# Optimization experiments

Hardware: AMD Instinct MI355X
Metric: run time of the kernel (lower is better)

## Reference

```python
import jax, jax.numpy as jnp
import numpy as np

NUM_HEADS = 8
NUM_LANDMARKS = 64
TOPK_LANDMARKS = 4


def setup_inputs() -> dict:
    key = jax.random.key(0)
    k1, k2, k3, k4 = jax.random.split(key, 4)
    B, N, C = 1, 2048, 512
    return {
        "x": jax.random.normal(k1, (B, N, C), jnp.float32),
        "w_qkv": jax.random.normal(k2, (3 * C, C), jnp.float32) * 0.02,
        "w_proj": jax.random.normal(k3, (C, C), jnp.float32) * 0.02,
        "b_proj": jax.random.normal(k4, (C,), jnp.float32) * 0.02,
    }


def reference(x, w_qkv, w_proj, b_proj):
    B, N, C = x.shape
    H = NUM_HEADS
    Dh = C // H
    m = min(NUM_LANDMARKS, N)          # number of segments (torch views (B,H,m,seg,D))
    kl = min(TOPK_LANDMARKS, m)
    scale = Dh ** -0.5

    qkv = (x @ w_qkv.T).reshape(B, N, 3, H, Dh).transpose(2, 0, 3, 1, 4)
    q, k, v = qkv[0], qkv[1], qkv[2]   # each (B,H,N,Dh)

    seg = -(-N // m)                   # segment length = ceil(N/m)
    pad = seg * m - N

    def segmentize(t):
        if pad > 0:
            t = jnp.pad(t, ((0, 0), (0, 0), (0, pad), (0, 0)))
        return t.reshape(B, H, m, seg, Dh)

    k_seg = segmentize(k)              # (B,H,m,seg,Dh)
    v_seg = segmentize(v)

    centroids = k_seg.mean(axis=3)     # (B,H,m,Dh) -- includes pad zeros, as in torch
    route = jnp.einsum('bhnd,bhmd->bhnm', q, centroids) * scale
    _, topk_idx = jax.lax.top_k(route, kl)  # (B,H,N,kl)

    # gather routed segments per query: (B,H,N,kl,seg,Dh)
    gather = jax.vmap(jax.vmap(lambda segs, ix: segs[ix]))
    sel_k = gather(k_seg, topk_idx).reshape(B, H, N, kl * seg, Dh)
    sel_v = gather(v_seg, topk_idx).reshape(B, H, N, kl * seg, Dh)

    attn = jnp.einsum('bhnd,bhnkd->bhnk', q, sel_k) * scale
    attn = jax.nn.softmax(attn, axis=-1)
    out = jnp.einsum('bhnk,bhnkd->bhnd', attn, sel_v)  # (B,H,N,Dh)
    out = out.transpose(0, 2, 1, 3).reshape(B, N, C)
    return out @ w_proj.T + b_proj
```

## Files before the change

kernel.cpp:

```cpp
#include <hip/hip_runtime.h>
#include <hip/hip_bf16.h>
#include <math.h>

#define N_TOK 2048
#define C_DIM 512
#define H_NUM 8
#define DH 64
#define M_LM 64
#define SEG 32
#define KL 4
#define SCALE 0.125f

typedef __attribute__((ext_vector_type(8))) short short8;
typedef __attribute__((ext_vector_type(8))) unsigned short ushort8v;
typedef __attribute__((ext_vector_type(4))) float f32x4;

__device__ inline unsigned short f2bf(float f) {
  unsigned u = __float_as_uint(f);
  u += 0x7FFF + ((u >> 16) & 1);
  return (unsigned short)(u >> 16);
}
__device__ inline float bf2f(unsigned short h) {
  return __uint_as_float(((unsigned)h) << 16);
}

__global__ __launch_bounds__(256) void gemm_qk(
    const float* __restrict__ A, const float* __restrict__ B,
    float* __restrict__ out_q, float* __restrict__ out_k,
    unsigned short* __restrict__ kbf)
{
  __shared__ float As[2][32][68];
  __shared__ float Bs[2][32][68];
  int tid = threadIdx.x;
  int tx = tid & 15, ty = tid >> 4;
  int row0 = blockIdx.y << 6;
  int col0 = blockIdx.x << 6;
  float acc[4][4] = {};
  int kk = tid & 31, rr = tid >> 5;

  float pa[8], pb[8];
#pragma unroll
  for (int i = 0; i < 8; i++) {
    pa[i] = A[(size_t)(row0 + rr + i * 8) * 512 + kk];
    pb[i] = B[(size_t)(col0 + rr + i * 8) * 512 + kk];
  }
#pragma unroll
  for (int i = 0; i < 8; i++) {
    As[0][kk][rr + i * 8] = pa[i];
    Bs[0][kk][rr + i * 8] = pb[i];
  }
  __syncthreads();

  for (int t = 0; t < 16; t++) {
    int cur = t & 1;
    if (t + 1 < 16) {
#pragma unroll
      for (int i = 0; i < 8; i++) {
        pa[i] = A[(size_t)(row0 + rr + i * 8) * 512 + (t + 1) * 32 + kk];
        pb[i] = B[(size_t)(col0 + rr + i * 8) * 512 + (t + 1) * 32 + kk];
      }
    }
#pragma unroll
    for (int kk2 = 0; kk2 < 32; kk2++) {
      float a[4], b[4];
      *(float4*)a = *(const float4*)&As[cur][kk2][ty << 2];
      *(float4*)b = *(const float4*)&Bs[cur][kk2][tx << 2];
#pragma unroll
      for (int i = 0; i < 4; i++)
#pragma unroll
        for (int j = 0; j < 4; j++) acc[i][j] += a[i] * b[j];
    }
    if (t + 1 < 16) {
#pragma unroll
      for (int i = 0; i < 8; i++) {
        As[cur ^ 1][kk][rr + i * 8] = pa[i];
        Bs[cur ^ 1][kk][rr + i * 8] = pb[i];
      }
    }
    __syncthreads();
  }

  int t = col0 >> 9;
  int h = (col0 >> 6) & 7;
  float* dst = (t == 0) ? out_q : out_k;
#pragma unroll
  for (int i = 0; i < 4; i++) {
    int n = row0 + (ty << 2) + i;
#pragma unroll
    for (int j = 0; j < 4; j++) {
      int d = (tx << 2) + j;
      float v = acc[i][j];
      dst[(size_t)((h << 11) + n) * DH + d] = v;
      if (t == 1) kbf[(size_t)((h << 11) + n) * DH + d] = f2bf(v);
    }
  }
}

__global__ void split3_kernel(const float* __restrict__ x, const float* __restrict__ wv,
                              const float* __restrict__ wp,
                              unsigned short* __restrict__ X2,
                              unsigned short* __restrict__ W2v,
                              unsigned short* __restrict__ WP2)
{
  int idx = blockIdx.x * 256 + threadIdx.x;
  const float* src; unsigned short* dst; int li;
  if (idx < 1048576)      { src = x;  dst = X2;  li = idx; }
  else if (idx < 1310720) { src = wv; dst = W2v; li = idx - 1048576; }
  else                    { src = wp; dst = WP2; li = idx - 1310720; }
  int r = li >> 9, k = li & 511;
  float a = src[li];
  unsigned short h1 = f2bf(a);
  float r1 = a - bf2f(h1);
  dst[(size_t)(r << 10) + k] = h1;
  dst[(size_t)(r << 10) + 512 + k] = f2bf(r1);
}

__global__ __launch_bounds__(256) void gemm_mfma(
    const unsigned short* __restrict__ A2, const unsigned short* __restrict__ B2,
    unsigned short* __restrict__ ov16, float* __restrict__ ofull,
    const float* __restrict__ bias, int ldout, int mode)
{
  __shared__ short Al[4096];
  __shared__ short Bl[4096];
  int tid = threadIdx.x;
  int lane = tid & 63, w = tid >> 6;
  int row0 = blockIdx.y << 6, col0 = blockIdx.x << 6;
  int wr = (w >> 1) * 32, wc = (w & 1) * 32;
  int m_lo = tid & 7, h8 = (tid >> 3) & 7, m_hi = tid >> 6;
  int ms = m_hi * 8 + m_lo;
  int q = lane >> 4, ln = lane & 15;

  f32x4 acc[2][2];
#pragma unroll
  for (int mi = 0; mi < 2; mi++)
#pragma unroll
    for (int ni = 0; ni < 2; ni++)
#pragma unroll
      for (int r = 0; r < 4; r++) acc[mi][ni][r] = 0.0f;

  for (int s = 0; s < 24; s++) {
    int ka = (s < 8) ? s * 64 : (s < 16) ? 512 + (s - 8) * 64 : (s - 16) * 64;
    int kb = (s < 8) ? s * 64 : (s < 16) ? (s - 8) * 64 : 512 + (s - 16) * 64;
    short8 a0 = *(const short8*)(A2 + (size_t)(row0 + ms) * 1024 + ka + h8 * 8);
    short8 a1 = *(const short8*)(A2 + (size_t)(row0 + ms + 32) * 1024 + ka + h8 * 8);
    short8 b0 = *(const short8*)(B2 + (size_t)(col0 + ms) * 1024 + kb + h8 * 8);
    short8 b1 = *(const short8*)(B2 + (size_t)(col0 + ms + 32) * 1024 + kb + h8 * 8);
    __syncthreads();
    *(short8*)&Al[(h8 * 64 + ms) * 8] = a0;
    *(short8*)&Al[(h8 * 64 + ms + 32) * 8] = a1;
    *(short8*)&Bl[(h8 * 64 + ms) * 8] = b0;
    *(short8*)&Bl[(h8 * 64 + ms + 32) * 8] = b1;
    __syncthreads();
    short8 af[2][2], bf[2][2];
#pragma unroll
    for (int sub = 0; sub < 2; sub++)
#pragma unroll
      for (int i = 0; i < 2; i++) {
        af[sub][i] = *(const short8*)&Al[((sub * 4 + q) * 64 + wr + i * 16 + ln) * 8];
        bf[sub][i] = *(const short8*)&Bl[((sub * 4 + q) * 64 + wc + i * 16 + ln) * 8];
      }
#pragma unroll
    for (int sub = 0; sub < 2; sub++)
#pragma unroll
      for (int mi = 0; mi < 2; mi++)
#pragma unroll
        for (int ni = 0; ni < 2; ni++)
          acc[mi][ni] = __builtin_amdgcn_mfma_f32_16x16x32_bf16(
              af[sub][mi], bf[sub][ni], acc[mi][ni], 0, 0, 0);
  }

  if (mode == 0) {
    int hh = (col0 >> 6) & 7;
#pragma unroll
    for (int mi = 0; mi < 2; mi++)
#pragma unroll
      for (int ni = 0; ni < 2; ni++)
#pragma unroll
        for (int r = 0; r < 4; r++) {
          int row = row0 + wr + mi * 16 + q * 4 + r;
          int d = wc + ni * 16 + ln;
          ov16[(size_t)((hh << 11) + row) * DH + d] = f2bf(acc[mi][ni][r]);
        }
  } else {
#pragma unroll
    for (int mi = 0; mi < 2; mi++)
#pragma unroll
      for (int ni = 0; ni < 2; ni++)
#pragma unroll
        for (int r = 0; r < 4; r++) {
          int row = row0 + wr + mi * 16 + q * 4 + r;
          int col = col0 + wc + ni * 16 + ln;
          ofull[(size_t)row * ldout + col] = acc[mi][ni][r] + bias[col];
        }
  }
}

__global__ void centroid_kernel(const float* __restrict__ kb, float* __restrict__ cent)
{
  int idx = blockIdx.x * blockDim.x + threadIdx.x;
  int m = (idx >> 6) & 63;
  int h = idx >> 12;
  int d = idx & 63;
  const float* base = kb + ((size_t)(h << 11) + m * SEG) * DH + d;
  float s = 0.f;
#pragma unroll
  for (int ss = 0; ss < SEG; ss++) s += base[(size_t)ss * DH];
  cent[idx] = s * (1.0f / SEG);
}

__global__ __launch_bounds__(256) void route_topk_kernel(
    const float* __restrict__ qb, const float* __restrict__ cent, int* __restrict__ topk)
{
  __shared__ float centT[64][65];
  __shared__ float qs[4][64];
  int tid = threadIdx.x;
  int wave = tid >> 6, lane = tid & 63;
  int qi = (blockIdx.x << 2) + wave;
  int h = qi >> 11;
  qs[wave][lane] = qb[(size_t)qi * DH + lane];
  const float4* c4 = (const float4*)(cent + ((size_t)h << 12));
#pragma unroll
  for (int i = 0; i < 4; i++) {
    int f4 = tid + 256 * i;
    int m = f4 >> 4;
    int d0 = (f4 & 15) * 4;
    float4 v = c4[f4];
    centT[d0][m] = v.x; centT[d0 + 1][m] = v.y;
    centT[d0 + 2][m] = v.z; centT[d0 + 3][m] = v.w;
  }
  __syncthreads();
  float dot = 0.f;
#pragma unroll
  for (int d = 0; d < 64; d++) dot += qs[wave][d] * centT[d][lane];
  float val = dot * SCALE;
  for (int r = 0; r < KL; r++) {
    float v = val;
    int id = lane;
#pragma unroll
    for (int off = 32; off; off >>= 1) {
      float ov = __shfl_xor(v, off, 64);
      int oi = __shfl_xor(id, off, 64);
      if (ov > v || (ov == v && oi < id)) { v = ov; id = oi; }
    }
    if (lane == 0) topk[qi * KL + r] = id;
    if (lane == id) val = -INFINITY;
  }
}

__global__ __launch_bounds__(256) void attn_kernel(
    const float* __restrict__ qb, const unsigned short* __restrict__ kbf,
    const unsigned short* __restrict__ vbf, const int* __restrict__ topk,
    unsigned short* __restrict__ ao2)
{
  __shared__ float probs[4][132];
  int tid = threadIdx.x;
  int wave = tid >> 6, lane = tid & 63;
  int qi = (blockIdx.x << 2) + wave;
  int h = qi >> 11, n = qi & 2047;
  int4 tk = *(const int4*)(topk + qi * KL);
  int segArr[4] = {tk.x, tk.y, tk.z, tk.w};
  const float* qrow = qb + (size_t)qi * DH;
  float4 qreg[4];
#pragma unroll
  for (int j = 0; j < 2; j++) {
    qreg[j * 2]     = *(const float4*)(qrow + ((lane & 3) + 4 * j) * 8);
    qreg[j * 2 + 1] = *(const float4*)(qrow + ((lane & 3) + 4 * j) * 8 + 4);
  }

  float e[8];
  float score[8];
#pragma unroll
  for (int g = 0; g < 8; g++) {
    int seg = segArr[g >> 1];
    int key_n = seg * SEG + (lane >> 2) + 16 * (g & 1);
    const unsigned short* krow = kbf + ((size_t)(h << 11) + key_n) * DH;
    float a0 = 0.f, a1 = 0.f, a2 = 0.f, a3 = 0.f;
#pragma unroll
    for (int j = 0; j < 2; j++) {
      ushort8v kv = *(const ushort8v*)(krow + ((lane & 3) + 4 * j) * 8);
      float4 q0 = qreg[j * 2], q1 = qreg[j * 2 + 1];
      a0 += q0.x * bf2f(kv[0]); a1 += q0.y * bf2f(kv[1]);
      a2 += q0.z * bf2f(kv[2]); a3 += q0.w * bf2f(kv[3]);
      a0 += q1.x * bf2f(kv[4]); a1 += q1.y * bf2f(kv[5]);
      a2 += q1.z * bf2f(kv[6]); a3 += q1.w * bf2f(kv[7]);
    }
    float acc = (a0 + a1) + (a2 + a3);
    acc += __shfl_xor(acc, 1, 64);
    acc += __shfl_xor(acc, 2, 64);
    score[g] = acc * SCALE;
  }
  float mx = score[0];
#pragma unroll
  for (int g = 1; g < 8; g++) mx = fmaxf(mx, score[g]);
#pragma unroll
  for (int off = 4; off < 64; off <<= 1) mx = fmaxf(mx, __shfl_xor(mx, off, 64));
  float ls = 0.f;
#pragma unroll
  for (int g = 0; g < 8; g++) { e[g] = expf(score[g] - mx); ls += e[g]; }
#pragma unroll
  for (int off = 4; off < 64; off <<= 1) ls += __shfl_xor(ls, off, 64);
  float inv = 1.0f / ls;
  if ((lane & 3) == 0) {
#pragma unroll
    for (int g = 0; g < 8; g++)
      probs[wave][(g >> 1) * 33 + (lane >> 2) + 16 * (g & 1)] = e[g] * inv;
  }
  __syncthreads();

  int gi = lane >> 4, lx = lane & 15;
  int rh = lx >> 3, dl = lx & 7;
  int seg = segArr[gi];
  const unsigned short* vbase = vbf + ((size_t)(h << 11) + seg * SEG) * DH + dl * 8;
  float o[8] = {};
#pragma unroll
  for (int ss = 0; ss < 16; ss++) {
    int row = rh * 16 + ss;
    float p = probs[wave][gi * 33 + row];
    ushort8v vv = *(const ushort8v*)(vbase + (size_t)row * DH);
#pragma unroll
    for (int j = 0; j < 8; j++) o[j] += p * bf2f(vv[j]);
  }
#pragma unroll
  for (int off = 8; off < 64; off <<= 1) {
#pragma unroll
    for (int j = 0; j < 8; j++) o[j] += __shfl_xor(o[j], off, 64);
  }
  if (lane < 8) {
    ushort8v hi8, lo8;
#pragma unroll
    for (int j = 0; j < 8; j++) {
      unsigned short hb = f2bf(o[j]);
      hi8[j] = (short)hb;
      lo8[j] = (short)f2bf(o[j] - bf2f(hb));
    }
    *(ushort8v*)(ao2 + (size_t)n * 1024 + (h << 6) + (lane << 3)) = hi8;
    *(ushort8v*)(ao2 + (size_t)n * 1024 + 512 + (h << 6) + (lane << 3)) = lo8;
  }
}

extern "C" void kernel_launch(void* const* d_in, const int* in_sizes, int n_in,
                              void* d_out, int out_size, void* d_ws, size_t ws_size,
                              hipStream_t stream)
{
  const float* x      = (const float*)d_in[0];
  const float* w_qkv  = (const float*)d_in[1];
  const float* w_proj = (const float*)d_in[2];
  const float* b_proj = (const float*)d_in[3];
  float* out = (float*)d_out;

  float* base = (float*)d_ws;
  float* qbuf = base;
  float* kbuf = base + 1048576;
  unsigned short* vbf = (unsigned short*)(base + 2097152);
  unsigned short* kbf = (unsigned short*)(base + 2621440);
  float* cent = base + 3145728;
  int*   topk = (int*)(base + 3178496);
  unsigned short* X2  = (unsigned short*)(base + 3244032);
  unsigned short* W2v = (unsigned short*)(base + 4292608);
  unsigned short* WP2 = (unsigned short*)(base + 4554752);
  unsigned short* AO2 = X2;

  split3_kernel<<<6144, 256, 0, stream>>>(x, w_qkv + 1024 * 512, w_proj,
                                          X2, W2v, WP2);
  {
    dim3 grid(1024 / 64, N_TOK / 64);
    gemm_qk<<<grid, 256, 0, stream>>>(x, w_qkv, qbuf, kbuf, kbf);
  }
  {
    dim3 grid(512 / 64, N_TOK / 64);
    gemm_mfma<<<grid, 256, 0, stream>>>(X2, W2v, vbf, nullptr, nullptr, 0, 0);
  }
  centroid_kernel<<<(H_NUM * M_LM * DH) / 256, 256, 0, stream>>>(kbuf, cent);
  route_topk_kernel<<<(H_NUM * N_TOK) / 4, 256, 0, stream>>>(qbuf, cent, topk);
  attn_kernel<<<(H_NUM * N_TOK) / 4, 256, 0, stream>>>(qbuf, kbf, vbf, topk, AO2);
  {
    dim3 grid(C_DIM / 64, N_TOK / 64);
    gemm_mfma<<<grid, 256, 0, stream>>>(AO2, WP2, nullptr, out, b_proj, C_DIM, 1);
  }
}
```

Measured before the change: 210.7 us.

## Pre-transpose QK GEMM inputs and stage tiles via direct global-to-LDS loads

Adds a transpose kernel that writes x and the Q/K weight rows into K-major layouts. The fp32 QK GEMM can then fill its shared-memory tiles with global_load_lds 16-byte transfers instead of strided scalar loads and register staging. The intent is to cut the uncoalesced load cost and the register round trip in the GEMM. In exchange it adds an extra kernel launch, extra memory traffic for the transposed copies, and workspace use. It also removes the LDS padding, which may cause bank conflicts.

```diff
diff --git a/kernel.cpp b/kernel.cpp
--- a/kernel.cpp
+++ b/kernel.cpp
@@ -24,42 +24,74 @@
   return __uint_as_float(((unsigned)h) << 16);
 }
 
+#define GLDS(g, l)                                                    \
+  __builtin_amdgcn_global_load_lds(                                   \
+      (const __attribute__((address_space(1))) void*)(g),             \
+      (__attribute__((address_space(3))) void*)(l), 16, 0, 0)
+
+__global__ __launch_bounds__(256) void transpose_kernel(
+    const float* __restrict__ x, const float* __restrict__ wq,
+    float* __restrict__ xT, float* __restrict__ wT)
+{
+  __shared__ float T[64][65];
+  int b = blockIdx.x;
+  const float* src; float* dst; int br, bc, R;
+  if (b < 256) { src = x;  dst = xT; br = (b >> 3) << 6; bc = (b & 7) << 6; R = 2048; }
+  else { int b2 = b - 256; src = wq; dst = wT; br = (b2 >> 3) << 6; bc = (b2 & 7) << 6; R = 1024; }
+  int tid = threadIdx.x;
+  int r0 = tid >> 4, c0 = (tid & 15) << 2;
+#pragma unroll
+  for (int i = 0; i < 4; i++) {
+    float4 v = *(const float4*)(src + (size_t)(br + r0 + i * 16) * 512 + bc + c0);
+    T[c0 + 0][r0 + i * 16] = v.x;
+    T[c0 + 1][r0 + i * 16] = v.y;
+    T[c0 + 2][r0 + i * 16] = v.z;
+    T[c0 + 3][r0 + i * 16] = v.w;
+  }
+  __syncthreads();
+#pragma unroll
+  for (int i = 0; i < 4; i++) {
+    float4 o;
+    o.x = T[r0 + i * 16][c0 + 0];
+    o.y = T[r0 + i * 16][c0 + 1];
+    o.z = T[r0 + i * 16][c0 + 2];
+    o.w = T[r0 + i * 16][c0 + 3];
+    *(float4*)(dst + (size_t)(bc + r0 + i * 16) * R + br + c0) = o;
+  }
+}
+
 __global__ __launch_bounds__(256) void gemm_qk(
-    const float* __restrict__ A, const float* __restrict__ B,
+    const float* __restrict__ AT, const float* __restrict__ BT,
     float* __restrict__ out_q, float* __restrict__ out_k,
     unsigned short* __restrict__ kbf)
 {
-  __shared__ float As[2][32][68];
-  __shared__ float Bs[2][32][68];
+  __shared__ __align__(16) float As[2][32][64];
+  __shared__ __align__(16) float Bs[2][32][64];
   int tid = threadIdx.x;
   int tx = tid & 15, ty = tid >> 4;
   int row0 = blockIdx.y << 6;
   int col0 = blockIdx.x << 6;
+  int w = tid >> 6, lane = tid & 63;
+  int lr = lane >> 4, lc = (lane & 15) << 2;
   float acc[4][4] = {};
-  int kk = tid & 31, rr = tid >> 5;
-
-  float pa[8], pb[8];
-#pragma unroll
-  for (int i = 0; i < 8; i++) {
-    pa[i] = A[(size_t)(row0 + rr + i * 8) * 512 + kk];
-    pb[i] = B[(size_t)(col0 + rr + i * 8) * 512 + kk];
-  }
-#pragma unroll
-  for (int i = 0; i < 8; i++) {
-    As[0][kk][rr + i * 8] = pa[i];
-    Bs[0][kk][rr + i * 8] = pb[i];
-  }
+
+#define STAGE(buf, t)                                                        \
+  {                                                                          \
+    _Pragma("unroll") for (int c = 0; c < 2; c++) {                          \
+      int kr = w * 8 + c * 4;                                                \
+      GLDS(AT + (size_t)((t) * 32 + kr + lr) * 2048 + row0 + lc,             \
+           &As[buf][kr][0]);                                                 \
+      GLDS(BT + (size_t)((t) * 32 + kr + lr) * 1024 + col0 + lc,             \
+           &Bs[buf][kr][0]);                                                 \
+    }                                                                        \
+  }
+
+  STAGE(0, 0);
   __syncthreads();
 
   for (int t = 0; t < 16; t++) {
     int cur = t & 1;
-    if (t + 1 < 16) {
-#pragma unroll
-      for (int i = 0; i < 8; i++) {
-        pa[i] = A[(size_t)(row0 + rr + i * 8) * 512 + (t + 1) * 32 + kk];
-        pb[i] = B[(size_t)(col0 + rr + i * 8) * 512 + (t + 1) * 32 + kk];
-      }
-    }
+    if (t + 1 < 16) STAGE(cur ^ 1, t + 1);
 #pragma unroll
     for (int kk2 = 0; kk2 < 32; kk2++) {
       float a[4], b[4];
@@ -70,19 +102,13 @@
 #pragma unroll
         for (int j = 0; j < 4; j++) acc[i][j] += a[i] * b[j];
     }
-    if (t + 1 < 16) {
-#pragma unroll
-      for (int i = 0; i < 8; i++) {
-        As[cur ^ 1][kk][rr + i * 8] = pa[i];
-        Bs[cur ^ 1][kk][rr + i * 8] = pb[i];
-      }
-    }
     __syncthreads();
   }
-
-  int t = col0 >> 9;
+#undef STAGE
+
+  int role = col0 >> 9;
   int h = (col0 >> 6) & 7;
-  float* dst = (t == 0) ? out_q : out_k;
+  float* dst = (role == 0) ? out_q : out_k;
 #pragma unroll
   for (int i = 0; i < 4; i++) {
     int n = row0 + (ty << 2) + i;
@@ -91,7 +117,7 @@
       int d = (tx << 2) + j;
       float v = acc[i][j];
       dst[(size_t)((h << 11) + n) * DH + d] = v;
-      if (t == 1) kbf[(size_t)((h << 11) + n) * DH + d] = f2bf(v);
+      if (role == 1) kbf[(size_t)((h << 11) + n) * DH + d] = f2bf(v);
     }
   }
 }
@@ -358,14 +384,17 @@
   unsigned short* X2  = (unsigned short*)(base + 3244032);
   unsigned short* W2v = (unsigned short*)(base + 4292608);
   unsigned short* WP2 = (unsigned short*)(base + 4554752);
+  float* xT = base + 4816896;
+  float* wT = base + 5865472;
   unsigned short* AO2 = X2;
 
+  transpose_kernel<<<384, 256, 0, stream>>>(x, w_qkv, xT, wT);
+  {
+    dim3 grid(1024 / 64, N_TOK / 64);
+    gemm_qk<<<grid, 256, 0, stream>>>(xT, wT, qbuf, kbuf, kbf);
+  }
   split3_kernel<<<6144, 256, 0, stream>>>(x, w_qkv + 1024 * 512, w_proj,
                                           X2, W2v, WP2);
-  {
-    dim3 grid(1024 / 64, N_TOK / 64);
-    gemm_qk<<<grid, 256, 0, stream>>>(x, w_qkv, qbuf, kbuf, kbf);
-  }
   {
     dim3 grid(512 / 64, N_TOK / 64);
     gemm_mfma<<<grid, 256, 0, stream>>>(X2, W2v, vbf, nullptr, nullptr, 0, 0);
```

After: 215.9 us. +2.5%, slower.
